# Kernel optimization log

Hardware: AMD Instinct MI355X
Metric: run time of the kernel (lower is better)

## Reference

```python
import jax, jax.numpy as jnp
import numpy as np
from jax import lax

BLOCK_LEN = 128  # ctx_len 8192 / blocks 64
NEG_INF = -1e9


def setup_inputs() -> dict:
    key = jax.random.key(0)
    ks = jax.random.split(key, 8)
    N, L, Dm = 2, 8192, 4096
    W, H, dh = 1024, 16, 64  # width = d_model*0.25
    s = lambda fan: 1.0 / np.sqrt(fan)
    return {
        "inputs": jax.random.normal(ks[0], (N, L, Dm), jnp.float32),
        "conv_w": jax.random.normal(ks[1], (3, Dm, 3 * W), jnp.float32) * s(3 * Dm),
        "conv_b": jnp.zeros((3 * W,), jnp.float32),
        "wq": jax.random.normal(ks[2], (W, H, dh), jnp.float32) * s(W),
        "bq": jnp.zeros((H, dh), jnp.float32),
        "wk": jax.random.normal(ks[3], (W, H, dh), jnp.float32) * s(W),
        "bk": jnp.zeros((H, dh), jnp.float32),
        "wv": jax.random.normal(ks[4], (W, H, dh), jnp.float32) * s(W),
        "bv": jnp.zeros((H, dh), jnp.float32),
        "wo": jax.random.normal(ks[5], (H, dh, W), jnp.float32) * s(H * dh),
        "bo": jnp.zeros((W,), jnp.float32),
        "proj_w": jax.random.normal(ks[6], (W, Dm), jnp.float32) * s(W),
        "proj_b": jnp.zeros((Dm,), jnp.float32),
    }


def reference(inputs, conv_w, conv_b, wq, bq, wk, bk, wv, bv, wo, bo, proj_w, proj_b):
    N, L, Dm = inputs.shape
    # Conv1D(kernel=3, same padding) producing q,k,v concatenated
    x = lax.conv_general_dilated(
        inputs, conv_w, window_strides=(1,), padding="SAME",
        dimension_numbers=("NWC", "WIO", "NWC")) + conv_b
    q, k, v = jnp.split(x, 3, axis=-1)  # each [N, L, W]
    W_ = q.shape[-1]
    nb = L // BLOCK_LEN
    # row attention: independent causal attention within each block
    q = q.reshape(N * nb, BLOCK_LEN, W_)
    k = k.reshape(N * nb, BLOCK_LEN, W_)
    v = v.reshape(N * nb, BLOCK_LEN, W_)
    dh = wq.shape[-1]
    qh = jnp.einsum("btd,dhe->bthe", q, wq) + bq  # [B, T, H, dh]
    kh = jnp.einsum("btd,dhe->bthe", k, wk) + bk
    vh = jnp.einsum("btd,dhe->bthe", v, wv) + bv
    scale = 1.0 / jnp.sqrt(jnp.asarray(dh, qh.dtype))
    scores = jnp.einsum("bqhe,bkhe->bhqk", qh * scale, kh)
    causal = jnp.tril(jnp.ones((BLOCK_LEN, BLOCK_LEN), bool))
    scores = jnp.where(causal, scores, NEG_INF)
    p = jax.nn.softmax(scores, axis=-1)
    o = jnp.einsum("bhqk,bkhe->bqhe", p, vh)
    o = jnp.einsum("bqhe,hed->bqd", o, wo) + bo  # MHA output projection -> width
    o = o.reshape(N, L, W_)
    return o @ proj_w + proj_b  # final Dense(d_model)
```

## Files before the change

### kernel.cpp

```cpp
#include <hip/hip_runtime.h>
#include <hip/hip_bf16.h>
#include <stdint.h>

typedef __attribute__((ext_vector_type(8))) short short8;
typedef __attribute__((ext_vector_type(4))) float f32x4;

#define AS1 __attribute__((address_space(1)))
#define AS3 __attribute__((address_space(3)))

__device__ __forceinline__ short f2bf(float x) {
    __hip_bfloat16 h = __float2bfloat16(x);
    union { __hip_bfloat16 h; short s; } u; u.h = h; return u.s;
}

__device__ __forceinline__ void gload_lds16(const short* g, short* l) {
    __builtin_amdgcn_global_load_lds((const AS1 void*)g, (AS3 void*)l, 16, 0, 0);
}

#define SBAR()   __builtin_amdgcn_s_barrier()
#define WAITV(N) asm volatile("s_waitcnt vmcnt(" #N ")")
#define SCHED0() __builtin_amdgcn_sched_barrier(0)
#define VMCNT0_BAR() do { WAITV(0); SBAR(); SCHED0(); } while (0)

__global__ __launch_bounds__(512, 2) void conv3_gemm(
    const short* __restrict__ A,
    const short* __restrict__ BT,
    short* __restrict__ Cout,
    const float* __restrict__ bias)
{
    __shared__ __align__(16) short As[2 * 272 * 32];
    __shared__ __align__(16) short Bs[2 * 3 * 256 * 32];
    const int tid = threadIdx.x, lane = tid & 63, wid = tid >> 6;
    const int wm = wid >> 2, wn = wid & 3;
    const int m0 = blockIdx.y * 256, n0 = blockIdx.x * 256;
    const size_t arow0 = (size_t)(m0 >> 13) * 8194 + (size_t)(m0 & 8191);
    const short* Abase = A + arow0 * 4096;
    const short* Bbase = BT + (size_t)n0 * 4096;
    const int c15 = lane & 15, g = lane >> 4, g4 = g * 4;
    const int xr0 = (c15 >> 1) & 3;
    const int xr1 = ((c15 + 1) >> 1) & 3;
    const int xr2 = ((c15 + 2) >> 1) & 3;
    const int srow = tid >> 2;
    const int schunk = (((tid & 3) ^ ((tid >> 3) & 3)) * 8);
    const int srowX = lane >> 2;
    const int schunkX = (((lane & 3) ^ ((lane >> 3) & 3)) * 8);

#define STAGE(s, buf) do { \
    const int kc_ = (s) * 32; \
    const short* ga_ = Abase + (size_t)srow * 4096 + kc_ + schunk; \
    short* la_ = As + (buf) * 8704 + wid * 512; \
    gload_lds16(ga_, la_); \
    gload_lds16(ga_ + 128 * 4096, la_ + 4096); \
    if (wid == 7) \
        gload_lds16(Abase + (size_t)(256 + srowX) * 4096 + kc_ + schunkX, \
                    As + (buf) * 8704 + 256 * 32); \
    _Pragma("unroll") \
    for (int tp_ = 0; tp_ < 3; ++tp_) { \
        const short* gb_ = Bbase + (size_t)tp_ * 3072 * 4096 \
                           + (size_t)srow * 4096 + kc_ + schunk; \
        short* lb_ = Bs + (buf) * 24576 + tp_ * 8192 + wid * 512; \
        gload_lds16(gb_, lb_); \
        gload_lds16(gb_ + 128 * 4096, lb_ + 4096); \
    } \
} while (0)

#define LDA_T(buf, mi, T, XR) (*(const short8*)(As + (buf) * 8704 \
    + (wm * 128 + (mi) * 16 + c15 + (T)) * 32 + ((g ^ (XR)) * 8)))
#define LDB_T(buf, tp, nj) (*(const short8*)(Bs + (buf) * 24576 + (tp) * 8192 \
    + (wn * 64 + (nj) * 16 + c15) * 32 + ((g ^ xr0) * 8)))

    f32x4 acc[8][4];
    #pragma unroll
    for (int i = 0; i < 8; ++i)
        #pragma unroll
        for (int j = 0; j < 4; ++j)
            acc[i][j] = (f32x4){0.f, 0.f, 0.f, 0.f};

    STAGE(0, 0);

    for (int s = 0; s < 128; ++s) {
        const int c = s & 1;
        VMCNT0_BAR();
        if (s + 1 < 128) STAGE(s + 1, c ^ 1);
        #pragma unroll
        for (int tp = 0; tp < 3; ++tp) {
            const int xr = (tp == 0) ? xr0 : (tp == 1) ? xr1 : xr2;
            short8 b0 = LDB_T(c, tp, 0), b1 = LDB_T(c, tp, 1);
            short8 b2f = LDB_T(c, tp, 2), b3 = LDB_T(c, tp, 3);
            __builtin_amdgcn_s_setprio(1);
            #pragma unroll
            for (int mi = 0; mi < 8; ++mi) {
                short8 a = LDA_T(c, mi, tp, xr);
                acc[mi][0] = __builtin_amdgcn_mfma_f32_16x16x32_bf16(a, b0, acc[mi][0], 0, 0, 0);
                acc[mi][1] = __builtin_amdgcn_mfma_f32_16x16x32_bf16(a, b1, acc[mi][1], 0, 0, 0);
                acc[mi][2] = __builtin_amdgcn_mfma_f32_16x16x32_bf16(a, b2f, acc[mi][2], 0, 0, 0);
                acc[mi][3] = __builtin_amdgcn_mfma_f32_16x16x32_bf16(a, b3, acc[mi][3], 0, 0, 0);
            }
            __builtin_amdgcn_s_setprio(0);
        }
    }

    float bv[4];
    #pragma unroll
    for (int nj = 0; nj < 4; ++nj)
        bv[nj] = bias[n0 + wn * 64 + nj * 16 + c15];
    #pragma unroll
    for (int mi = 0; mi < 8; ++mi) {
        #pragma unroll
        for (int r = 0; r < 4; ++r) {
            const size_t row = (size_t)m0 + wm * 128 + mi * 16 + g4 + r;
            #pragma unroll
            for (int nj = 0; nj < 4; ++nj) {
                const int col = n0 + wn * 64 + nj * 16 + c15;
                Cout[row * 3072 + col] = f2bf(acc[mi][nj][r] + bv[nj]);
            }
        }
    }
#undef STAGE
#undef LDA_T
#undef LDB_T
}

template<int MODE, bool F32OUT>
__global__ __launch_bounds__(512, 2) void gemm256(
    const short* __restrict__ A, int lda,
    const short* __restrict__ BT, int ldb,
    void* __restrict__ Cout, int ldc,
    const float* __restrict__ bias, int Ktiles)
{
    __shared__ __align__(16) short As[2 * 2 * 256 * 32];
    __shared__ __align__(16) short Bs[2 * 2 * 256 * 32];
    const int tid = threadIdx.x, lane = tid & 63, wid = tid >> 6;
    const int wm = wid >> 2, wn = wid & 3;
    const int m0 = blockIdx.y * 256, n0 = blockIdx.x * 256;
    const size_t ldaS = (size_t)lda, ldbS = (size_t)ldb;
    const short* Abase0 = A + (size_t)m0 * ldaS;
    const short* Bbase0 = BT + (size_t)n0 * ldbS + ((MODE == 1) ? (m0 & ~1023) : 0);
    const int c15 = lane & 15, g4 = (lane >> 4) * 4;
    const int swz = ((lane >> 4) ^ ((c15 >> 1) & 3)) * 8;
    const int srow = tid >> 2;
    const int schunk = (((tid & 3) ^ ((tid >> 3) & 3)) * 8);

#define STG_A(u, kh, buf) do { \
    const short* g_ = Abase0 + ((u) << 6) + (kh) * 32 + (size_t)srow * ldaS + schunk; \
    short* l_ = As + (buf) * 16384 + (kh) * 8192 + wid * 512; \
    gload_lds16(g_, l_); \
    gload_lds16(g_ + 128 * ldaS, l_ + 4096); \
} while (0)

#define STG_B(u, kh, buf) do { \
    const short* g_ = Bbase0 + ((u) << 6) + (kh) * 32 + (size_t)srow * ldbS + schunk; \
    short* l_ = Bs + (buf) * 16384 + (kh) * 8192 + wid * 512; \
    gload_lds16(g_, l_); \
    gload_lds16(g_ + 128 * ldbS, l_ + 4096); \
} while (0)

#define LDA_(buf, kk, mi) (*(const short8*)(As + (buf) * 16384 + (kk) * 8192 \
                           + (wm * 128 + (mi) * 16 + c15) * 32 + swz))
#define LDB_(buf, kk, nj) (*(const short8*)(Bs + (buf) * 16384 + (kk) * 8192 \
                           + (wn * 64 + (nj) * 16 + c15) * 32 + swz))

#define MFMA4x4(MB) do { \
    __builtin_amdgcn_s_setprio(1); \
    _Pragma("unroll") \
    for (int mi_ = 0; mi_ < 4; ++mi_) \
        _Pragma("unroll") \
        for (int nj_ = 0; nj_ < 4; ++nj_) \
            acc[(MB) + mi_][nj_] = __builtin_amdgcn_mfma_f32_16x16x32_bf16( \
                af[mi_], bf4[nj_], acc[(MB) + mi_][nj_], 0, 0, 0); \
    __builtin_amdgcn_s_setprio(0); \
} while (0)

    f32x4 acc[8][4];
    #pragma unroll
    for (int i = 0; i < 8; ++i)
        #pragma unroll
        for (int j = 0; j < 4; ++j)
            acc[i][j] = (f32x4){0.f, 0.f, 0.f, 0.f};

    STG_A(0, 0, 0); STG_B(0, 0, 0); STG_A(0, 1, 0); STG_B(0, 1, 0);
    WAITV(4); SBAR(); SCHED0();

    for (int t = 0; t < Ktiles; ++t) {
        const int c = t & 1, nb = c ^ 1;
        const bool st = (t + 1 < Ktiles);
        const int u = t + 1;
        short8 af[4], bf4[4];

        #pragma unroll
        for (int mi = 0; mi < 4; ++mi) af[mi] = LDA_(c, 0, mi);
        #pragma unroll
        for (int nj = 0; nj < 4; ++nj) bf4[nj] = LDB_(c, 0, nj);
        if (st) STG_A(u, 0, nb);
        SBAR();
        MFMA4x4(0);
        SBAR();

        #pragma unroll
        for (int mi = 0; mi < 4; ++mi) af[mi] = LDA_(c, 0, 4 + mi);
        if (st) STG_B(u, 0, nb);
        if (st) { WAITV(4); } else { WAITV(0); }
        SBAR(); SCHED0();
        MFMA4x4(4);
        SBAR();

        #pragma unroll
        for (int mi = 0; mi < 4; ++mi) af[mi] = LDA_(c, 1, mi);
        #pragma unroll
        for (int nj = 0; nj < 4; ++nj) bf4[nj] = LDB_(c, 1, nj);
        if (st) STG_A(u, 1, nb);
        SBAR();
        MFMA4x4(0);
        SBAR();

        #pragma unroll
        for (int mi = 0; mi < 4; ++mi) af[mi] = LDA_(c, 1, 4 + mi);
        if (st) STG_B(u, 1, nb);
        if (st) { WAITV(4); } else { WAITV(0); }
        SBAR(); SCHED0();
        MFMA4x4(4);
        SBAR();
    }

    float bv[4];
    #pragma unroll
    for (int nj = 0; nj < 4; ++nj)
        bv[nj] = bias ? bias[n0 + wn * 64 + nj * 16 + c15] : 0.f;
    #pragma unroll
    for (int mi = 0; mi < 8; ++mi) {
        #pragma unroll
        for (int r = 0; r < 4; ++r) {
            const size_t row = (size_t)m0 + wm * 128 + mi * 16 + g4 + r;
            #pragma unroll
            for (int nj = 0; nj < 4; ++nj) {
                const int col = n0 + wn * 64 + nj * 16 + c15;
                const float v = acc[mi][nj][r] + bv[nj];
                if (F32OUT) ((float*)Cout)[row * (size_t)ldc + col] = v;
                else        ((short*)Cout)[row * (size_t)ldc + col] = f2bf(v);
            }
        }
    }
#undef STG_A
#undef STG_B
#undef LDA_
#undef LDB_
#undef MFMA4x4
}

__global__ __launch_bounds__(256) void attn_kernel(
    const short* __restrict__ qkvh, short* __restrict__ obuf)
{
    __shared__ __align__(16) char smem[54272];
    short* qs = (short*)smem;
    short* ks = (short*)smem + 9216;
    short* vt = (short*)(smem + 36864);
    short* ps = (short*)smem;
    short* os = (short*)smem;

    const int tid = threadIdx.x, lane = tid & 63, wid = tid >> 6;
    const int h = blockIdx.x, b = blockIdx.y;
    const size_t base = (size_t)b * 128 * 3072 + (size_t)h * 64;

    for (int i = tid; i < 1024; i += 256) {
        const int row = i >> 3, c8 = i & 7;
        const size_t g = base + (size_t)row * 3072 + c8 * 8;
        *(short8*)(qs + row * 72 + c8 * 8) = *(const short8*)(qkvh + g);
        *(short8*)(ks + row * 72 + c8 * 8) = *(const short8*)(qkvh + g + 1024);
        short8 vv = *(const short8*)(qkvh + g + 2048);
        #pragma unroll
        for (int j = 0; j < 8; ++j) vt[(c8 * 8 + j) * 136 + row] = vv[j];
    }
    __syncthreads();

    const int c15 = lane & 15, g8 = (lane >> 4) * 8, g4 = (lane >> 4) * 4;
    const int r0 = wid * 32;

    f32x4 sacc[2][8];
    #pragma unroll
    for (int mi = 0; mi < 2; ++mi)
        #pragma unroll
        for (int nj = 0; nj < 8; ++nj)
            sacc[mi][nj] = (f32x4){0.f, 0.f, 0.f, 0.f};
    #pragma unroll
    for (int kk = 0; kk < 2; ++kk) {
        short8 aq[2];
        #pragma unroll
        for (int mi = 0; mi < 2; ++mi)
            aq[mi] = *(const short8*)(qs + (r0 + mi * 16 + c15) * 72 + kk * 32 + g8);
        #pragma unroll
        for (int nj = 0; nj < 8; ++nj) {
            short8 bk8 = *(const short8*)(ks + (nj * 16 + c15) * 72 + kk * 32 + g8);
            #pragma unroll
            for (int mi = 0; mi < 2; ++mi)
                sacc[mi][nj] = __builtin_amdgcn_mfma_f32_16x16x32_bf16(
                    aq[mi], bk8, sacc[mi][nj], 0, 0, 0);
        }
    }
    __syncthreads();

    #pragma unroll
    for (int mi = 0; mi < 2; ++mi) {
        #pragma unroll
        for (int r = 0; r < 4; ++r) {
            const int qrow = r0 + mi * 16 + g4 + r;
            float m = -3.0e38f, pv[8];
            #pragma unroll
            for (int nj = 0; nj < 8; ++nj) {
                float s = sacc[mi][nj][r] * 0.125f;
                if (nj * 16 + c15 > qrow) s = -1.0e9f;
                pv[nj] = s; m = fmaxf(m, s);
            }
            #pragma unroll
            for (int off = 8; off >= 1; off >>= 1) m = fmaxf(m, __shfl_xor(m, off));
            float sum = 0.f;
            #pragma unroll
            for (int nj = 0; nj < 8; ++nj) { float p = __expf(pv[nj] - m); pv[nj] = p; sum += p; }
            #pragma unroll
            for (int off = 8; off >= 1; off >>= 1) sum += __shfl_xor(sum, off);
            const float inv = 1.0f / sum;
            #pragma unroll
            for (int nj = 0; nj < 8; ++nj)
                ps[qrow * 136 + nj * 16 + c15] = f2bf(pv[nj] * inv);
        }
    }
    __syncthreads();

    f32x4 oacc[2][4];
    #pragma unroll
    for (int mi = 0; mi < 2; ++mi)
        #pragma unroll
        for (int nj = 0; nj < 4; ++nj)
            oacc[mi][nj] = (f32x4){0.f, 0.f, 0.f, 0.f};
    #pragma unroll
    for (int kt = 0; kt < 4; ++kt) {
        short8 ap[2];
        #pragma unroll
        for (int mi = 0; mi < 2; ++mi)
            ap[mi] = *(const short8*)(ps + (r0 + mi * 16 + c15) * 136 + kt * 32 + g8);
        #pragma unroll
        for (int nj = 0; nj < 4; ++nj) {
            short8 bv8 = *(const short8*)(vt + (nj * 16 + c15) * 136 + kt * 32 + g8);
            #pragma unroll
            for (int mi = 0; mi < 2; ++mi)
                oacc[mi][nj] = __builtin_amdgcn_mfma_f32_16x16x32_bf16(
                    ap[mi], bv8, oacc[mi][nj], 0, 0, 0);
        }
    }
    __syncthreads();

    #pragma unroll
    for (int mi = 0; mi < 2; ++mi)
        #pragma unroll
        for (int r = 0; r < 4; ++r)
            #pragma unroll
            for (int nj = 0; nj < 4; ++nj)
                os[(r0 + mi * 16 + g4 + r) * 72 + nj * 16 + c15] = f2bf(oacc[mi][nj][r]);
    __syncthreads();

    for (int i = tid; i < 1024; i += 256) {
        const int row = i >> 3, c8 = i & 7;
        *(short8*)(obuf + (size_t)b * 128 * 1024 + (size_t)h * 64
                   + (size_t)row * 1024 + c8 * 8) =
            *(const short8*)(os + row * 72 + c8 * 8);
    }
}

__global__ void pad_convert_inputs(const float* __restrict__ in, short* __restrict__ out)
{
    const int row = blockIdx.x;
    const int n = row / 8194, l = row % 8194;
    short* orow = out + (size_t)row * 4096;
    if (l == 0 || l == 8193) {
        for (int i = threadIdx.x; i < 512; i += 256) {
            uint4 z; z.x = z.y = z.z = z.w = 0u;
            *(uint4*)(orow + i * 8) = z;
        }
    } else {
        const float* irow = in + ((size_t)n * 8192 + (l - 1)) * 4096;
        for (int i = threadIdx.x; i < 512; i += 256) {
            float4 a = *(const float4*)(irow + i * 8);
            float4 b = *(const float4*)(irow + i * 8 + 4);
            short8 v;
            v[0] = f2bf(a.x); v[1] = f2bf(a.y); v[2] = f2bf(a.z); v[3] = f2bf(a.w);
            v[4] = f2bf(b.x); v[5] = f2bf(b.y); v[6] = f2bf(b.z); v[7] = f2bf(b.w);
            *(short8*)(orow + i * 8) = v;
        }
    }
}

__global__ void transpose_convert(const float* __restrict__ in, short* __restrict__ out,
                                  int R, int C)
{
    __shared__ float tile[32][33];
    const int tx = threadIdx.x & 31, ty = threadIdx.x >> 5;
    const int bx = blockIdx.x * 32, by = blockIdx.y * 32;
    #pragma unroll
    for (int i = 0; i < 32; i += 8)
        tile[ty + i][tx] = in[(size_t)(by + ty + i) * C + bx + tx];
    __syncthreads();
    #pragma unroll
    for (int i = 0; i < 32; i += 8)
        out[(size_t)(bx + ty + i) * R + by + tx] = f2bf(tile[tx][ty + i]);
}

__global__ void convert_bf16(const float* __restrict__ in, short* __restrict__ out, int n8)
{
    const int idx = blockIdx.x * 256 + threadIdx.x;
    if (idx < n8) {
        float4 a = *(const float4*)(in + (size_t)idx * 8);
        float4 b = *(const float4*)(in + (size_t)idx * 8 + 4);
        short8 v;
        v[0] = f2bf(a.x); v[1] = f2bf(a.y); v[2] = f2bf(a.z); v[3] = f2bf(a.w);
        v[4] = f2bf(b.x); v[5] = f2bf(b.y); v[6] = f2bf(b.z); v[7] = f2bf(b.w);
        *(short8*)(out + (size_t)idx * 8) = v;
    }
}

__global__ void fuse_bias(const float* __restrict__ bo, const float* __restrict__ projw,
                          const float* __restrict__ projb, float* __restrict__ outb)
{
    const int j = blockIdx.x * 256 + threadIdx.x;
    float s = projb[j];
    for (int w = 0; w < 1024; ++w) s = fmaf(bo[w], projw[(size_t)w * 4096 + j], s);
    outb[j] = s;
}

__global__ void fuse_bias_qkv(const float* __restrict__ conv_b,
                              const float* __restrict__ wq, const float* __restrict__ bq,
                              const float* __restrict__ wk, const float* __restrict__ bk,
                              const float* __restrict__ wv, const float* __restrict__ bv,
                              float* __restrict__ outb)
{
    const int o = blockIdx.x * 256 + threadIdx.x;
    const int p = o >> 10, e = o & 1023;
    const float* w = (p == 0) ? wq : (p == 1) ? wk : wv;
    const float* bb = (p == 0) ? bq : (p == 1) ? bk : bv;
    const float* cb = conv_b + p * 1024;
    float s = bb[e];
    for (int d = 0; d < 1024; ++d) s = fmaf(cb[d], w[(size_t)d * 1024 + e], s);
    outb[o] = s;
}

extern "C" void kernel_launch(void* const* d_in, const int* in_sizes, int n_in,
                              void* d_out, int out_size, void* d_ws, size_t ws_size,
                              hipStream_t stream)
{
    const float* inputs = (const float*)d_in[0];
    const float* conv_w = (const float*)d_in[1];
    const float* conv_b = (const float*)d_in[2];
    const float* wq     = (const float*)d_in[3];
    const float* bq     = (const float*)d_in[4];
    const float* wk     = (const float*)d_in[5];
    const float* bk     = (const float*)d_in[6];
    const float* wv     = (const float*)d_in[7];
    const float* bv     = (const float*)d_in[8];
    const float* wo     = (const float*)d_in[9];
    const float* bo     = (const float*)d_in[10];
    const float* proj_w = (const float*)d_in[11];
    const float* proj_b = (const float*)d_in[12];

    char* ws = (char*)d_ws;
    short* in_pad = (short*)(ws + 0);
    short* cw_bf  = (short*)(ws + 134283264);
    short* qkvh   = (short*)(ws + 134283264);
    short* W2T    = (short*)(ws + 234946560);
    short* wq_t   = (short*)(ws + 310444032);
    short* wo_bf  = (short*)(ws + 316735488);
    short* proj_t = (short*)(ws + 318832640);
    short* WfT    = (short*)(ws + 327221248);
    float* bfused = (float*)(ws + 335609856);
    float* b2     = (float*)(ws + 335626240);
    short* o_buf  = (short*)(ws + 0);

    dim3 blk(256), blk5(512);

    pad_convert_inputs<<<16388, blk, 0, stream>>>(inputs, in_pad);
    convert_bf16<<<18432, blk, 0, stream>>>(conv_w, cw_bf, 4718592);
    transpose_convert<<<dim3(32, 32), blk, 0, stream>>>(wq, wq_t, 1024, 1024);
    transpose_convert<<<dim3(32, 32), blk, 0, stream>>>(wk, wq_t + 1048576, 1024, 1024);
    transpose_convert<<<dim3(32, 32), blk, 0, stream>>>(wv, wq_t + 2097152, 1024, 1024);
    transpose_convert<<<dim3(128, 32), blk, 0, stream>>>(proj_w, proj_t, 1024, 4096);
    convert_bf16<<<512, blk, 0, stream>>>(wo, wo_bf, 131072);
    fuse_bias<<<16, blk, 0, stream>>>(bo, proj_w, proj_b, bfused);
    fuse_bias_qkv<<<12, blk, 0, stream>>>(conv_b, wq, bq, wk, bk, wv, bv, b2);

    gemm256<0, false><<<dim3(4, 16), blk5, 0, stream>>>(
        proj_t, 1024, wo_bf, 1024, WfT, 1024, nullptr, 16);
    for (int t = 0; t < 3; ++t)
        gemm256<1, false><<<dim3(16, 12), blk5, 0, stream>>>(
            wq_t, 1024, cw_bf + (size_t)t * 4096 * 3072, 3072,
            W2T + (size_t)t * 3072 * 4096, 4096, nullptr, 16);
    conv3_gemm<<<dim3(12, 64), blk5, 0, stream>>>(in_pad, W2T, qkvh, b2);

    attn_kernel<<<dim3(16, 128), blk, 0, stream>>>(qkvh, o_buf);

    gemm256<0, true><<<dim3(16, 64), blk5, 0, stream>>>(
        o_buf, 1024, WfT, 1024, d_out, 4096, bfused, 16);
}
```

Measured before the change: 1.598 ms.

## Shrink conv3 GEMM tile to 256x128 single-buffered with 256 threads

The conv3 GEMM moves from a 256x256 tile with 512 threads and double-buffered LDS to a 256x128 tile with 256 threads and a single LDS buffer. Loads are now issued after compute, behind an extra barrier. The goal is less LDS per block so three blocks can share a CU, and twice as many blocks in the grid. The cost is that loads no longer overlap compute inside a block, so latency hiding depends on other resident blocks. The A tile is also re-read for each N tile, which adds global traffic.

```diff
diff --git a/kernel.cpp b/kernel.cpp
--- a/kernel.cpp
+++ b/kernel.cpp
@@ -20,19 +20,18 @@
 #define SBAR()   __builtin_amdgcn_s_barrier()
 #define WAITV(N) asm volatile("s_waitcnt vmcnt(" #N ")")
 #define SCHED0() __builtin_amdgcn_sched_barrier(0)
-#define VMCNT0_BAR() do { WAITV(0); SBAR(); SCHED0(); } while (0)
-
-__global__ __launch_bounds__(512, 2) void conv3_gemm(
+
+__global__ __launch_bounds__(256, 3) void conv3_gemm(
     const short* __restrict__ A,
     const short* __restrict__ BT,
     short* __restrict__ Cout,
     const float* __restrict__ bias)
 {
-    __shared__ __align__(16) short As[2 * 272 * 32];
-    __shared__ __align__(16) short Bs[2 * 3 * 256 * 32];
+    __shared__ __align__(16) short As[258 * 32];
+    __shared__ __align__(16) short Bs[3 * 128 * 32];
     const int tid = threadIdx.x, lane = tid & 63, wid = tid >> 6;
-    const int wm = wid >> 2, wn = wid & 3;
-    const int m0 = blockIdx.y * 256, n0 = blockIdx.x * 256;
+    const int wm = wid >> 1, wn = wid & 1;
+    const int m0 = blockIdx.y * 256, n0 = blockIdx.x * 128;
     const size_t arow0 = (size_t)(m0 >> 13) * 8194 + (size_t)(m0 & 8191);
     const short* Abase = A + arow0 * 4096;
     const short* Bbase = BT + (size_t)n0 * 4096;
@@ -42,31 +41,33 @@
     const int xr2 = ((c15 + 2) >> 1) & 3;
     const int srow = tid >> 2;
     const int schunk = (((tid & 3) ^ ((tid >> 3) & 3)) * 8);
-    const int srowX = lane >> 2;
-    const int schunkX = (((lane & 3) ^ ((lane >> 3) & 3)) * 8);
-
-#define STAGE(s, buf) do { \
+    const int srowB = wid * 32 + (lane >> 2);
+    const int schunkB = (((lane & 3) ^ ((lane >> 3) & 3)) * 8);
+
+#define STAGE(s) do { \
     const int kc_ = (s) * 32; \
     const short* ga_ = Abase + (size_t)srow * 4096 + kc_ + schunk; \
-    short* la_ = As + (buf) * 8704 + wid * 512; \
+    short* la_ = As + wid * 512; \
     gload_lds16(ga_, la_); \
-    gload_lds16(ga_ + 128 * 4096, la_ + 4096); \
-    if (wid == 7) \
-        gload_lds16(Abase + (size_t)(256 + srowX) * 4096 + kc_ + schunkX, \
-                    As + (buf) * 8704 + 256 * 32); \
+    gload_lds16(ga_ + (size_t)64 * 4096, la_ + 2048); \
+    gload_lds16(ga_ + (size_t)128 * 4096, la_ + 4096); \
+    gload_lds16(ga_ + (size_t)192 * 4096, la_ + 6144); \
+    if (wid == 3 && lane < 8) \
+        gload_lds16(Abase + (size_t)(256 + (lane >> 2)) * 4096 + kc_ + (lane & 3) * 8, \
+                    As + 8192); \
     _Pragma("unroll") \
     for (int tp_ = 0; tp_ < 3; ++tp_) { \
         const short* gb_ = Bbase + (size_t)tp_ * 3072 * 4096 \
-                           + (size_t)srow * 4096 + kc_ + schunk; \
-        short* lb_ = Bs + (buf) * 24576 + tp_ * 8192 + wid * 512; \
+                           + (size_t)srowB * 4096 + kc_ + schunkB; \
+        short* lb_ = Bs + tp_ * 4096 + wid * 1024; \
         gload_lds16(gb_, lb_); \
-        gload_lds16(gb_ + 128 * 4096, lb_ + 4096); \
+        gload_lds16(gb_ + (size_t)16 * 4096, lb_ + 512); \
     } \
 } while (0)
 
-#define LDA_T(buf, mi, T, XR) (*(const short8*)(As + (buf) * 8704 \
+#define LDA_T(mi, T, XR) (*(const short8*)(As \
     + (wm * 128 + (mi) * 16 + c15 + (T)) * 32 + ((g ^ (XR)) * 8)))
-#define LDB_T(buf, tp, nj) (*(const short8*)(Bs + (buf) * 24576 + (tp) * 8192 \
+#define LDB_T(tp, nj) (*(const short8*)(Bs + (tp) * 4096 \
     + (wn * 64 + (nj) * 16 + c15) * 32 + ((g ^ xr0) * 8)))
 
     f32x4 acc[8][4];
@@ -76,21 +77,19 @@
         for (int j = 0; j < 4; ++j)
             acc[i][j] = (f32x4){0.f, 0.f, 0.f, 0.f};
 
-    STAGE(0, 0);
+    STAGE(0);
 
     for (int s = 0; s < 128; ++s) {
-        const int c = s & 1;
-        VMCNT0_BAR();
-        if (s + 1 < 128) STAGE(s + 1, c ^ 1);
+        WAITV(0); SBAR(); SCHED0();
         #pragma unroll
         for (int tp = 0; tp < 3; ++tp) {
             const int xr = (tp == 0) ? xr0 : (tp == 1) ? xr1 : xr2;
-            short8 b0 = LDB_T(c, tp, 0), b1 = LDB_T(c, tp, 1);
-            short8 b2f = LDB_T(c, tp, 2), b3 = LDB_T(c, tp, 3);
+            short8 b0 = LDB_T(tp, 0), b1 = LDB_T(tp, 1);
+            short8 b2f = LDB_T(tp, 2), b3 = LDB_T(tp, 3);
             __builtin_amdgcn_s_setprio(1);
             #pragma unroll
             for (int mi = 0; mi < 8; ++mi) {
-                short8 a = LDA_T(c, mi, tp, xr);
+                short8 a = LDA_T(mi, tp, xr);
                 acc[mi][0] = __builtin_amdgcn_mfma_f32_16x16x32_bf16(a, b0, acc[mi][0], 0, 0, 0);
                 acc[mi][1] = __builtin_amdgcn_mfma_f32_16x16x32_bf16(a, b1, acc[mi][1], 0, 0, 0);
                 acc[mi][2] = __builtin_amdgcn_mfma_f32_16x16x32_bf16(a, b2f, acc[mi][2], 0, 0, 0);
@@ -98,6 +97,8 @@
             }
             __builtin_amdgcn_s_setprio(0);
         }
+        SBAR();
+        if (s + 1 < 128) STAGE(s + 1);
     }
 
     float bv[4];
@@ -490,7 +491,7 @@
         gemm256<1, false><<<dim3(16, 12), blk5, 0, stream>>>(
             wq_t, 1024, cw_bf + (size_t)t * 4096 * 3072, 3072,
             W2T + (size_t)t * 3072 * 4096, 4096, nullptr, 16);
-    conv3_gemm<<<dim3(12, 64), blk5, 0, stream>>>(in_pad, W2T, qkvh, b2);
+    conv3_gemm<<<dim3(24, 64), blk, 0, stream>>>(in_pad, W2T, qkvh, b2);
 
     attn_kernel<<<dim3(16, 128), blk, 0, stream>>>(qkvh, o_buf);
 
```

Result: faster. 1.494 ms (-6.5%).
